# Optimization experiments

Hardware: AMD Instinct MI355X
Metric: run time of the kernel (lower is better)

The kernel has to match this reference:

```python
import jax, jax.numpy as jnp
import numpy as np

B, S, E = 2, 2048, 2048
NQ, NKV, HD = 16, 4, 128
WINDOW = 512
ROPE_BASE = 10000.0


def _rope(x):
    # x: [B, H, S, HD], interleaved even/odd rotation
    half = HD // 2
    freqs = 1.0 / (ROPE_BASE ** (2.0 * jnp.arange(half, dtype=jnp.float32) / HD))
    pos = jnp.arange(x.shape[2], dtype=jnp.float32)
    ang = pos[:, None] * freqs[None, :]            # [S, HD/2]
    cos = jnp.cos(ang)[None, None].astype(x.dtype)  # [1,1,S,HD/2]
    sin = jnp.sin(ang)[None, None].astype(x.dtype)
    xe = x[..., 0::2]
    xo = x[..., 1::2]
    re = xe * cos - xo * sin
    ro = xe * sin + xo * cos
    return jnp.stack([re, ro], axis=-1).reshape(x.shape)


def setup_inputs() -> dict:
    key = jax.random.key(0)
    ks = jax.random.split(key, 9)
    s_in = 1.0 / np.sqrt(E)
    s_out = 1.0 / np.sqrt(NQ * HD)
    return {
        "x": jax.random.normal(ks[0], (B, S, E), jnp.float32),
        "Wq": jax.random.normal(ks[1], (E, NQ * HD), jnp.float32) * s_in,
        "bq": jax.random.normal(ks[2], (NQ * HD,), jnp.float32) * 0.01,
        "Wk": jax.random.normal(ks[3], (E, NKV * HD), jnp.float32) * s_in,
        "bk": jax.random.normal(ks[4], (NKV * HD,), jnp.float32) * 0.01,
        "Wv": jax.random.normal(ks[5], (E, NKV * HD), jnp.float32) * s_in,
        "bv": jax.random.normal(ks[6], (NKV * HD,), jnp.float32) * 0.01,
        "Wo": jax.random.normal(ks[7], (NQ * HD, E), jnp.float32) * s_out,
        "bo": jax.random.normal(ks[8], (E,), jnp.float32) * 0.01,
    }


def reference(x, Wq, bq, Wk, bk, Wv, bv, Wo, bo):
    b, s, _ = x.shape
    q = (x @ Wq + bq).reshape(b, s, NQ, HD).transpose(0, 2, 1, 3)   # [B,NQ,S,HD]
    k = (x @ Wk + bk).reshape(b, s, NKV, HD).transpose(0, 2, 1, 3)  # [B,NKV,S,HD]
    v = (x @ Wv + bv).reshape(b, s, NKV, HD).transpose(0, 2, 1, 3)
    q = _rope(q)
    k = _rope(k)
    rep = NQ // NKV
    k = jnp.repeat(k, rep, axis=1)  # [B,NQ,S,HD], matches torch repeat pattern
    v = jnp.repeat(v, rep, axis=1)
    scores = jnp.einsum("bhqd,bhkd->bhqk", q, k) / np.sqrt(HD)
    i = jnp.arange(s)[:, None]
    j = jnp.arange(s)[None, :]
    allowed = (j <= i) & ((i - j) <= WINDOW)  # sliding-window causal mask
    scores = jnp.where(allowed[None, None], scores, -jnp.inf)
    weights = jax.nn.softmax(scores, axis=-1)
    out = jnp.einsum("bhqk,bhkd->bhqd", weights, v)
    out = out.transpose(0, 2, 1, 3).reshape(b, s, NQ * HD)
    return out @ Wo + bo
```

## Files before the change

### kernel.cpp

```cpp
#include <hip/hip_runtime.h>
#include <hip/hip_bf16.h>
#include <math.h>

#define BB 2
#define SS 2048
#define EE 2048
#define NQ 16
#define NKV 4
#define HD 128
#define WINDOW 512

typedef __hip_bfloat16 bf16;
typedef short short8 __attribute__((ext_vector_type(8)));
typedef float f32x4 __attribute__((ext_vector_type(4)));

__device__ __forceinline__ float toF(bf16 v) { return __bfloat162float(v); }
__device__ __forceinline__ bf16 toB(float v) { return __float2bfloat16(v); }

__device__ __forceinline__ void gld_lds16(const void* g, void* l) {
    __builtin_amdgcn_global_load_lds(
        (const __attribute__((address_space(1))) void*)g,
        (__attribute__((address_space(3))) void*)l, 16, 0, 0);
}

__global__ __launch_bounds__(256) void convert_bf16(const float* __restrict__ in,
                                                    bf16* __restrict__ out, int n) {
    int i = (blockIdx.x * 256 + threadIdx.x) * 4;
    if (i >= n) return;
    const float4 v = *(const float4*)(in + i);
    bf16 o[4] = {toB(v.x), toB(v.y), toB(v.z), toB(v.w)};
    *(uint2*)(out + i) = *(const uint2*)o;
}

__global__ __launch_bounds__(256) void convert_transpose(const float* __restrict__ in,
                                                         bf16* __restrict__ out,
                                                         int K, int N) {
    __shared__ float tile[32][33];
    const int t = threadIdx.x;
    const int tx = t & 31, ty = t >> 5;
    const int n0 = blockIdx.x * 32, k0 = blockIdx.y * 32;
#pragma unroll
    for (int r = 0; r < 4; r++)
        tile[ty + r * 8][tx] = in[(size_t)(k0 + ty + r * 8) * N + n0 + tx];
    __syncthreads();
#pragma unroll
    for (int r = 0; r < 4; r++)
        out[(size_t)(n0 + ty + r * 8) * K + k0 + tx] = toB(tile[tx][ty + r * 8]);
}

__global__ __launch_bounds__(256) void convert_transpose_qkv(
    const float* __restrict__ Wq, const float* __restrict__ Wk,
    const float* __restrict__ Wv, bf16* __restrict__ out) {
    __shared__ float tile[32][33];
    const int t = threadIdx.x;
    const int tx = t & 31, ty = t >> 5;
    const int n0 = blockIdx.x * 32, k0 = blockIdx.y * 32;
    const float* src; int N, nl0;
    if (n0 < 2048)      { src = Wq; N = 2048; nl0 = n0; }
    else if (n0 < 2560) { src = Wk; N = 512;  nl0 = n0 - 2048; }
    else                { src = Wv; N = 512;  nl0 = n0 - 2560; }
#pragma unroll
    for (int r = 0; r < 4; r++)
        tile[ty + r * 8][tx] = src[(size_t)(k0 + ty + r * 8) * N + nl0 + tx];
    __syncthreads();
#pragma unroll
    for (int r = 0; r < 4; r++)
        out[(size_t)(n0 + ty + r * 8) * 2048 + k0 + tx] = toB(tile[tx][ty + r * 8]);
}

__global__ __launch_bounds__(256) void v_transpose(const bf16* __restrict__ Vb,
                                                   bf16* __restrict__ Vtg) {
    __shared__ bf16 tile[64 * 72];
    const int t = threadIdx.x;
    const int s0 = blockIdx.x * 64;
    const int d0 = (blockIdx.y & 1) * 64;
    const int bh = blockIdx.y >> 1;
    const int b = bh >> 2, hkv = bh & 3;

    const bf16* src = Vb + (((size_t)b * SS + s0) * NKV + hkv) * HD + d0;
#pragma unroll
    for (int half = 0; half < 2; half++) {
        const int sl = (t >> 3) + half * 32;
        const int c  = t & 7;
        const int c2 = c ^ (sl & 7);
        short8 v = *(const short8*)(src + (size_t)sl * (NKV * HD) + c * 8);
        *(short8*)(&tile[sl * 72 + c2 * 8]) = v;
    }
    __syncthreads();

    const int d = t >> 2;
    const int sc = t & 3;
    bf16* dst = Vtg + (((size_t)b * NKV + hkv) * HD + d0 + d) * SS + s0 + sc * 16;
#pragma unroll
    for (int g = 0; g < 2; g++) {
        bf16 pk[8];
#pragma unroll
        for (int k = 0; k < 8; k++) {
            const int s = sc * 16 + g * 8 + k;
            const int c2 = (d >> 3) ^ (s & 7);
            pk[k] = tile[s * 72 + c2 * 8 + (d & 7)];
        }
        *(uint4*)(dst + g * 8) = *(const uint4*)pk;
    }
}

template <int MODE>
__global__ __launch_bounds__(256) void mfma_gemm(
    const bf16* __restrict__ A, const bf16* __restrict__ BT,
    const float* __restrict__ b0, const float* __restrict__ b1,
    const float* __restrict__ b2,
    float* __restrict__ Yf,
    bf16* __restrict__ Yq, bf16* __restrict__ Yk, bf16* __restrict__ Yv,
    int M, int N, int K) {
    __shared__ bf16 As[128 * 32];
    __shared__ bf16 Bs[128 * 32];

    const int t = threadIdx.x;
    const int lane = t & 63;
    const int w = t >> 6;
    const int wm = w >> 1, wn = w & 1;
    const int m0 = blockIdx.y * 128, n0 = blockIdx.x * 128;

    const int srow = lane >> 2;
    const int sg   = lane & 3;
    const int scol = (sg ^ ((srow >> 1) & 3)) * 8;

    f32x4 acc[4][4];
#pragma unroll
    for (int i = 0; i < 4; i++)
#pragma unroll
        for (int j = 0; j < 4; j++) acc[i][j] = (f32x4)0.f;

    const int lr = lane & 15;
    const int lq = lane >> 4;
    const int slotr = (lq ^ ((lr >> 1) & 3)) * 8;

    for (int k0 = 0; k0 < K; k0 += 32) {
#pragma unroll
        for (int s = 0; s < 2; s++) {
            const int c = w * 2 + s;
            gld_lds16(A + (size_t)(m0 + c * 16 + srow) * K + k0 + scol, As + c * 512);
            gld_lds16(BT + (size_t)(n0 + c * 16 + srow) * K + k0 + scol, Bs + c * 512);
        }
        __syncthreads();
        short8 af[4], bfv[4];
#pragma unroll
        for (int i = 0; i < 4; i++)
            af[i] = *(const short8*)(As + (wm * 64 + i * 16 + lr) * 32 + slotr);
#pragma unroll
        for (int j = 0; j < 4; j++)
            bfv[j] = *(const short8*)(Bs + (wn * 64 + j * 16 + lr) * 32 + slotr);
#pragma unroll
        for (int i = 0; i < 4; i++)
#pragma unroll
            for (int j = 0; j < 4; j++)
                acc[i][j] = __builtin_amdgcn_mfma_f32_16x16x32_bf16(af[i], bfv[j],
                                                                    acc[i][j], 0, 0, 0);
        __syncthreads();
    }

    if (MODE == 0) {
#pragma unroll
        for (int j = 0; j < 4; j++) {
            const int col = n0 + wn * 64 + j * 16 + lr;
            const float bj = b0[col];
#pragma unroll
            for (int i = 0; i < 4; i++) {
                const int row = m0 + wm * 64 + i * 16 + lq * 4;
#pragma unroll
                for (int r = 0; r < 4; r++)
                    Yf[(size_t)(row + r) * N + col] = acc[i][j][r] + bj;
            }
        }
    } else if (n0 < 2560) {
        bf16* outp; const float* bias; int ldc, c0; float oscale;
        if (n0 < 2048) { outp = Yq; bias = b0; ldc = 2048; c0 = n0;
                         oscale = 0.08838834764831845f; }
        else           { outp = Yk; bias = b1; ldc = 512;  c0 = n0 - 2048;
                         oscale = 1.0f; }
#pragma unroll
        for (int j = 0; j < 4; j++) {
            const int col = c0 + wn * 64 + j * 16 + lr;
            const float bj = bias[col];
            const int d2 = (col & 127) >> 1;
            const bool odd = col & 1;
            const float freq = __expf(-0.14384103622589045f * (float)d2);
#pragma unroll
            for (int i = 0; i < 4; i++) {
                const int row = m0 + wm * 64 + i * 16 + lq * 4;
#pragma unroll
                for (int r = 0; r < 4; r++) {
                    const float v = acc[i][j][r] + bj;
                    const float p = __shfl_xor(v, 1, 64);
                    const float ang = (float)((row + r) & (SS - 1)) * freq;
                    float sn, cs;
                    __sincosf(ang, &sn, &cs);
                    const float o = odd ? (p * sn + v * cs) : (v * cs - p * sn);
                    outp[(size_t)(row + r) * ldc + col] = toB(o * oscale);
                }
            }
        }
    } else {
        const int c0 = n0 - 2560;
#pragma unroll
        for (int j = 0; j < 4; j++) {
            const int col = c0 + wn * 64 + j * 16 + lr;
            const float bj = b2[col];
#pragma unroll
            for (int i = 0; i < 4; i++) {
                const int row = m0 + wm * 64 + i * 16 + lq * 4;
#pragma unroll
                for (int r = 0; r < 4; r++)
                    Yv[(size_t)(row + r) * 512 + col] = toB(acc[i][j][r] + bj);
            }
        }
    }
}

__global__ __launch_bounds__(256) void attn_mfma(const bf16* __restrict__ Q,
                                                 const bf16* __restrict__ K,
                                                 const bf16* __restrict__ Vt_g,
                                                 bf16* __restrict__ Oout) {
    __shared__ bf16 Ks[64 * 128];
    __shared__ bf16 Vt[128 * 64];
    __shared__ bf16 Ps[4 * 16 * 72];

    const int t = threadIdx.x;
    const int lane = t & 63;
    const int w = t >> 6;
    const int q0 = blockIdx.x * 64;
    const int h = blockIdx.y;
    const int b = blockIdx.z;
    const int hkv = h >> 2;
    const int lr = lane & 15;
    const int lq = lane >> 4;

    short8 aq[4];
    {
        const int q = q0 + w * 16 + lr;
        const bf16* qp = Q + (((size_t)b * SS + q) * NQ + h) * HD + lq * 8;
#pragma unroll
        for (int ks = 0; ks < 4; ks++) aq[ks] = *(const short8*)(qp + ks * 32);
    }

    f32x4 Oa[8];
#pragma unroll
    for (int nb = 0; nb < 8; nb++) Oa[nb] = (f32x4)0.f;
    float mprev[4] = {-3.0e38f, -3.0e38f, -3.0e38f, -3.0e38f};
    float lsum[4] = {0.f, 0.f, 0.f, 0.f};

    bf16* Pw = Ps + w * 16 * 72;
    const int jstart = (q0 >= WINDOW) ? (q0 - WINDOW) : 0;
    const bf16* Vrow = Vt_g + ((size_t)b * NKV + hkv) * HD * SS;

    for (int c0 = jstart; c0 <= q0; c0 += 64) {
        __syncthreads();
#pragma unroll
        for (int s = 0; s < 4; s++) {
            const int kr = w * 16 + s * 4 + (lane >> 4);
            const int sl = lane & 15;
            const int g = (sl & 8) | ((sl & 7) ^ (kr & 7));
            gld_lds16(K + (((size_t)b * SS + c0 + kr) * NKV + hkv) * HD + g * 8,
                      Ks + (w * 16 + s * 4) * 128);
        }
#pragma unroll
        for (int s = 0; s < 4; s++) {
            const int dr = w * 32 + s * 8 + (lane >> 3);
            const int sl = lane & 7;
            const int g = sl ^ (dr & 7);
            gld_lds16(Vrow + (size_t)dr * SS + c0 + g * 8,
                      Vt + (w * 32 + s * 8) * 64);
        }
        __syncthreads();

        f32x4 sa[4];
#pragma unroll
        for (int nb = 0; nb < 4; nb++) sa[nb] = (f32x4)0.f;
#pragma unroll
        for (int ks = 0; ks < 4; ks++) {
#pragma unroll
            for (int nb = 0; nb < 4; nb++) {
                const int row = nb * 16 + lr;
                const int g = ks * 4 + lq;
                const int slot = (g & 8) | ((g & 7) ^ (row & 7));
                short8 bk = *(const short8*)(Ks + row * 128 + slot * 8);
                sa[nb] = __builtin_amdgcn_mfma_f32_16x16x32_bf16(aq[ks], bk, sa[nb], 0, 0, 0);
            }
        }

        const int rowb = q0 + w * 16 + lq * 4;
        const bool needmask = !((c0 + 63 <= q0 + w * 16) &&
                                (q0 + w * 16 + 15 - c0 <= WINDOW));
        float pr[4][4], alpha[4];
#pragma unroll
        for (int r = 0; r < 4; r++) {
            const int row = rowb + r;
            float sv[4];
            float mx = -3.0e38f;
            if (needmask) {
#pragma unroll
                for (int nb = 0; nb < 4; nb++) {
                    const int col = c0 + nb * 16 + lr;
                    const bool valid = (col <= row) && (row - col <= WINDOW);
                    sv[nb] = valid ? sa[nb][r] : -3.0e38f;
                    mx = fmaxf(mx, sv[nb]);
                }
            } else {
#pragma unroll
                for (int nb = 0; nb < 4; nb++) {
                    sv[nb] = sa[nb][r];
                    mx = fmaxf(mx, sv[nb]);
                }
            }
#pragma unroll
            for (int off = 1; off < 16; off <<= 1) mx = fmaxf(mx, __shfl_xor(mx, off, 64));
            const float mn = fmaxf(fmaxf(mprev[r], mx), -1.0e30f);
            alpha[r] = __expf(mprev[r] - mn);
            mprev[r] = mn;
            float rs = 0.f;
#pragma unroll
            for (int nb = 0; nb < 4; nb++) {
                const float p = __expf(sv[nb] - mn);
                pr[r][nb] = p;
                rs += p;
            }
#pragma unroll
            for (int off = 1; off < 16; off <<= 1) rs += __shfl_xor(rs, off, 64);
            lsum[r] = lsum[r] * alpha[r] + rs;
        }

#pragma unroll
        for (int r = 0; r < 4; r++)
#pragma unroll
            for (int nb = 0; nb < 4; nb++)
                Pw[(lq * 4 + r) * 72 + nb * 16 + lr] = toB(pr[r][nb]);

#pragma unroll
        for (int nb = 0; nb < 8; nb++)
#pragma unroll
            for (int r = 0; r < 4; r++) Oa[nb][r] *= alpha[r];
#pragma unroll
        for (int ks = 0; ks < 2; ks++) {
            short8 pa = *(const short8*)(Pw + lr * 72 + ks * 32 + lq * 8);
#pragma unroll
            for (int nb = 0; nb < 8; nb++) {
                const int d = nb * 16 + lr;
                const int g = ks * 4 + lq;
                const int slot = g ^ (d & 7);
                short8 bv = *(const short8*)(Vt + d * 64 + slot * 8);
                Oa[nb] = __builtin_amdgcn_mfma_f32_16x16x32_bf16(pa, bv, Oa[nb], 0, 0, 0);
            }
        }
    }

    float linv[4];
#pragma unroll
    for (int r = 0; r < 4; r++) linv[r] = 1.f / lsum[r];
    const int rowb = q0 + w * 16 + lq * 4;
#pragma unroll
    for (int nb = 0; nb < 8; nb++)
#pragma unroll
        for (int r = 0; r < 4; r++)
            Oout[(((size_t)b * SS + rowb + r) * NQ + h) * HD + nb * 16 + lr] =
                toB(Oa[nb][r] * linv[r]);
}

extern "C" void kernel_launch(void* const* d_in, const int* in_sizes, int n_in,
                              void* d_out, int out_size, void* d_ws, size_t ws_size,
                              hipStream_t stream) {
    const float* x  = (const float*)d_in[0];
    const float* Wq = (const float*)d_in[1];
    const float* bq = (const float*)d_in[2];
    const float* Wk = (const float*)d_in[3];
    const float* bk = (const float*)d_in[4];
    const float* Wv = (const float*)d_in[5];
    const float* bv = (const float*)d_in[6];
    const float* Wo = (const float*)d_in[7];
    const float* bo = (const float*)d_in[8];
    float* out = (float*)d_out;

    const int M   = BB * SS;
    const int DQ  = NQ * HD;
    const int DKV = NKV * HD;
    const int NPK = DQ + 2 * DKV;

    bf16* xb     = (bf16*)d_ws;
    bf16* WqkvT  = xb + (size_t)M * EE;
    bf16* WoT    = WqkvT + (size_t)NPK * EE;
    bf16* Vb     = WoT;
    bf16* Qb     = WoT + (size_t)EE * DQ;
    bf16* Kb     = Qb + (size_t)M * DQ;
    bf16* Vtg    = Kb + (size_t)M * DKV;

    convert_bf16<<<(M * EE / 4 + 255) / 256, 256, 0, stream>>>(x, xb, M * EE);
    convert_transpose_qkv<<<dim3(NPK / 32, EE / 32), 256, 0, stream>>>(Wq, Wk, Wv, WqkvT);

    mfma_gemm<1><<<dim3(NPK / 128, M / 128), 256, 0, stream>>>(
        xb, WqkvT, bq, bk, bv, nullptr, Qb, Kb, Vb, M, NPK, EE);

    v_transpose<<<dim3(SS / 64, 2 * BB * NKV), 256, 0, stream>>>(Vb, Vtg);
    convert_transpose<<<dim3(DQ / 32, DQ / 32), 256, 0, stream>>>(Wo, WoT, DQ, EE);

    attn_mfma<<<dim3(SS / 64, NQ, BB), 256, 0, stream>>>(Qb, Kb, Vtg, Qb);

    mfma_gemm<0><<<dim3(EE / 128, M / 128), 256, 0, stream>>>(
        Qb, WoT, bo, nullptr, nullptr, out, nullptr, nullptr, nullptr, M, EE, DQ);
}
```

Before: 338.9 us.

## Use single-wave attention blocks reading K/V directly from global memory

The attention kernel changes from 256-thread blocks covering 64 query rows, which staged K and V tiles into shared memory with barriers, to 64-thread single-wavefront blocks covering 16 query rows. Each wave loads its K and V MFMA fragments straight from global memory, and the key-chunk start is aligned to 64. This removes __syncthreads and LDS staging and launches four times as many blocks for occupancy. In exchange, K/V reuse across the four waves is lost, so global/L2 traffic rises and the V fragment loads are strided.

Measured after the change: 463.5 us. 36.8% more time.

```diff
diff --git a/kernel.cpp b/kernel.cpp
--- a/kernel.cpp
+++ b/kernel.cpp
@@ -217,18 +217,14 @@
     }
 }
 
-__global__ __launch_bounds__(256) void attn_mfma(const bf16* __restrict__ Q,
-                                                 const bf16* __restrict__ K,
-                                                 const bf16* __restrict__ Vt_g,
-                                                 bf16* __restrict__ Oout) {
-    __shared__ bf16 Ks[64 * 128];
-    __shared__ bf16 Vt[128 * 64];
-    __shared__ bf16 Ps[4 * 16 * 72];
-
-    const int t = threadIdx.x;
-    const int lane = t & 63;
-    const int w = t >> 6;
-    const int q0 = blockIdx.x * 64;
+__global__ __launch_bounds__(64) void attn_mfma(const bf16* __restrict__ Q,
+                                                const bf16* __restrict__ K,
+                                                const bf16* __restrict__ Vt_g,
+                                                bf16* __restrict__ Oout) {
+    __shared__ bf16 Ps[16 * 72];
+
+    const int lane = threadIdx.x;
+    const int q0 = blockIdx.x * 16;
     const int h = blockIdx.y;
     const int b = blockIdx.z;
     const int hkv = h >> 2;
@@ -237,8 +233,7 @@
 
     short8 aq[4];
     {
-        const int q = q0 + w * 16 + lr;
-        const bf16* qp = Q + (((size_t)b * SS + q) * NQ + h) * HD + lq * 8;
+        const bf16* qp = Q + (((size_t)b * SS + q0 + lr) * NQ + h) * HD + lq * 8;
 #pragma unroll
         for (int ks = 0; ks < 4; ks++) aq[ks] = *(const short8*)(qp + ks * 32);
     }
@@ -249,48 +244,33 @@
     float mprev[4] = {-3.0e38f, -3.0e38f, -3.0e38f, -3.0e38f};
     float lsum[4] = {0.f, 0.f, 0.f, 0.f};
 
-    bf16* Pw = Ps + w * 16 * 72;
-    const int jstart = (q0 >= WINDOW) ? (q0 - WINDOW) : 0;
+    const bf16* Krow = K + ((size_t)b * SS * NKV + hkv) * HD;
     const bf16* Vrow = Vt_g + ((size_t)b * NKV + hkv) * HD * SS;
 
-    for (int c0 = jstart; c0 <= q0; c0 += 64) {
-        __syncthreads();
-#pragma unroll
-        for (int s = 0; s < 4; s++) {
-            const int kr = w * 16 + s * 4 + (lane >> 4);
-            const int sl = lane & 15;
-            const int g = (sl & 8) | ((sl & 7) ^ (kr & 7));
-            gld_lds16(K + (((size_t)b * SS + c0 + kr) * NKV + hkv) * HD + g * 8,
-                      Ks + (w * 16 + s * 4) * 128);
-        }
-#pragma unroll
-        for (int s = 0; s < 4; s++) {
-            const int dr = w * 32 + s * 8 + (lane >> 3);
-            const int sl = lane & 7;
-            const int g = sl ^ (dr & 7);
-            gld_lds16(Vrow + (size_t)dr * SS + c0 + g * 8,
-                      Vt + (w * 32 + s * 8) * 64);
-        }
-        __syncthreads();
-
+    int jstart = q0 - WINDOW;
+    if (jstart < 0) jstart = 0;
+    jstart &= ~63;
+
+    for (int c0 = jstart; c0 <= q0 + 15; c0 += 64) {
+        short8 bk[4][4];
+#pragma unroll
+        for (int nb = 0; nb < 4; nb++) {
+            const bf16* kp = Krow + (size_t)(c0 + nb * 16 + lr) * (NKV * HD) + lq * 8;
+#pragma unroll
+            for (int ks = 0; ks < 4; ks++) bk[ks][nb] = *(const short8*)(kp + ks * 32);
+        }
         f32x4 sa[4];
 #pragma unroll
         for (int nb = 0; nb < 4; nb++) sa[nb] = (f32x4)0.f;
 #pragma unroll
-        for (int ks = 0; ks < 4; ks++) {
-#pragma unroll
-            for (int nb = 0; nb < 4; nb++) {
-                const int row = nb * 16 + lr;
-                const int g = ks * 4 + lq;
-                const int slot = (g & 8) | ((g & 7) ^ (row & 7));
-                short8 bk = *(const short8*)(Ks + row * 128 + slot * 8);
-                sa[nb] = __builtin_amdgcn_mfma_f32_16x16x32_bf16(aq[ks], bk, sa[nb], 0, 0, 0);
-            }
-        }
-
-        const int rowb = q0 + w * 16 + lq * 4;
-        const bool needmask = !((c0 + 63 <= q0 + w * 16) &&
-                                (q0 + w * 16 + 15 - c0 <= WINDOW));
+        for (int ks = 0; ks < 4; ks++)
+#pragma unroll
+            for (int nb = 0; nb < 4; nb++)
+                sa[nb] = __builtin_amdgcn_mfma_f32_16x16x32_bf16(aq[ks], bk[ks][nb],
+                                                                 sa[nb], 0, 0, 0);
+
+        const int rowb = q0 + lq * 4;
+        const bool needmask = !((c0 + 63 <= q0) && (q0 + 15 - c0 <= WINDOW));
         float pr[4][4], alpha[4];
 #pragma unroll
         for (int r = 0; r < 4; r++) {
@@ -333,21 +313,19 @@
         for (int r = 0; r < 4; r++)
 #pragma unroll
             for (int nb = 0; nb < 4; nb++)
-                Pw[(lq * 4 + r) * 72 + nb * 16 + lr] = toB(pr[r][nb]);
+                Ps[(lq * 4 + r) * 72 + nb * 16 + lr] = toB(pr[r][nb]);
 
 #pragma unroll
         for (int nb = 0; nb < 8; nb++)
 #pragma unroll
             for (int r = 0; r < 4; r++) Oa[nb][r] *= alpha[r];
 #pragma unroll
-        for (int ks = 0; ks < 2; ks++) {
-            short8 pa = *(const short8*)(Pw + lr * 72 + ks * 32 + lq * 8);
+        for (int ks2 = 0; ks2 < 2; ks2++) {
+            short8 pa = *(const short8*)(Ps + lr * 72 + ks2 * 32 + lq * 8);
 #pragma unroll
             for (int nb = 0; nb < 8; nb++) {
-                const int d = nb * 16 + lr;
-                const int g = ks * 4 + lq;
-                const int slot = g ^ (d & 7);
-                short8 bv = *(const short8*)(Vt + d * 64 + slot * 8);
+                short8 bv = *(const short8*)(Vrow + (size_t)(nb * 16 + lr) * SS +
+                                             c0 + ks2 * 32 + lq * 8);
                 Oa[nb] = __builtin_amdgcn_mfma_f32_16x16x32_bf16(pa, bv, Oa[nb], 0, 0, 0);
             }
         }
@@ -356,7 +334,7 @@
     float linv[4];
 #pragma unroll
     for (int r = 0; r < 4; r++) linv[r] = 1.f / lsum[r];
-    const int rowb = q0 + w * 16 + lq * 4;
+    const int rowb = q0 + lq * 4;
 #pragma unroll
     for (int nb = 0; nb < 8; nb++)
 #pragma unroll
@@ -401,7 +379,7 @@
     v_transpose<<<dim3(SS / 64, 2 * BB * NKV), 256, 0, stream>>>(Vb, Vtg);
     convert_transpose<<<dim3(DQ / 32, DQ / 32), 256, 0, stream>>>(Wo, WoT, DQ, EE);
 
-    attn_mfma<<<dim3(SS / 64, NQ, BB), 256, 0, stream>>>(Qb, Kb, Vtg, Qb);
+    attn_mfma<<<dim3(SS / 16, NQ, BB), 64, 0, stream>>>(Qb, Kb, Vtg, Qb);
 
     mfma_gemm<0><<<dim3(EE / 128, M / 128), 256, 0, stream>>>(
         Qb, WoT, bo, nullptr, nullptr, out, nullptr, nullptr, nullptr, M, EE, DQ);
```

## Process 128 queries per attention block with two 16-row tiles per wave

Applied to the files above, without the earlier changes.

The attention kernel now handles 128 query rows per block, with each wave owning 32 rows as two 16-row MFMA tiles. Each K/V tile loaded into LDS is reused across twice as many queries, which roughly halves K/V global traffic and load/sync overhead per query. The cost is double the accumulator registers per wave, which can lower occupancy, and a grid half the size (512 blocks). Waves skip compute on chunks outside their own window, so they still join the shared loads but may sit idle for part of the loop.

Result: slower. 373.0 us (+10.1%).

```diff
diff --git a/kernel.cpp b/kernel.cpp
--- a/kernel.cpp
+++ b/kernel.cpp
@@ -223,37 +223,42 @@
                                                  bf16* __restrict__ Oout) {
     __shared__ bf16 Ks[64 * 128];
     __shared__ bf16 Vt[128 * 64];
-    __shared__ bf16 Ps[4 * 16 * 72];
+    __shared__ bf16 Ps[4 * 32 * 72];
 
     const int t = threadIdx.x;
     const int lane = t & 63;
     const int w = t >> 6;
-    const int q0 = blockIdx.x * 64;
+    const int q0 = blockIdx.x * 128;
     const int h = blockIdx.y;
     const int b = blockIdx.z;
     const int hkv = h >> 2;
     const int lr = lane & 15;
     const int lq = lane >> 4;
-
-    short8 aq[4];
-    {
-        const int q = q0 + w * 16 + lr;
-        const bf16* qp = Q + (((size_t)b * SS + q) * NQ + h) * HD + lq * 8;
-#pragma unroll
-        for (int ks = 0; ks < 4; ks++) aq[ks] = *(const short8*)(qp + ks * 32);
-    }
-
-    f32x4 Oa[8];
-#pragma unroll
-    for (int nb = 0; nb < 8; nb++) Oa[nb] = (f32x4)0.f;
-    float mprev[4] = {-3.0e38f, -3.0e38f, -3.0e38f, -3.0e38f};
-    float lsum[4] = {0.f, 0.f, 0.f, 0.f};
-
-    bf16* Pw = Ps + w * 16 * 72;
+    const int wq0 = q0 + w * 32;
+
+    short8 aq[2][4];
+#pragma unroll
+    for (int u = 0; u < 2; u++) {
+        const bf16* qp = Q + (((size_t)b * SS + wq0 + u * 16 + lr) * NQ + h) * HD + lq * 8;
+#pragma unroll
+        for (int ks = 0; ks < 4; ks++) aq[u][ks] = *(const short8*)(qp + ks * 32);
+    }
+
+    f32x4 Oa[2][8];
+#pragma unroll
+    for (int u = 0; u < 2; u++)
+#pragma unroll
+        for (int nb = 0; nb < 8; nb++) Oa[u][nb] = (f32x4)0.f;
+    float mprev[2][4], lsum[2][4];
+#pragma unroll
+    for (int u = 0; u < 2; u++)
+#pragma unroll
+        for (int r = 0; r < 4; r++) { mprev[u][r] = -3.0e38f; lsum[u][r] = 0.f; }
+
+    bf16* Pw = Ps + w * 32 * 72;
     const int jstart = (q0 >= WINDOW) ? (q0 - WINDOW) : 0;
-    const bf16* Vrow = Vt_g + ((size_t)b * NKV + hkv) * HD * SS;
-
-    for (int c0 = jstart; c0 <= q0; c0 += 64) {
+
+    for (int c0 = jstart; c0 < q0 + 128; c0 += 64) {
         __syncthreads();
 #pragma unroll
         for (int s = 0; s < 4; s++) {
@@ -268,14 +273,18 @@
             const int dr = w * 32 + s * 8 + (lane >> 3);
             const int sl = lane & 7;
             const int g = sl ^ (dr & 7);
-            gld_lds16(Vrow + (size_t)dr * SS + c0 + g * 8,
+            gld_lds16(Vt_g + (((size_t)b * NKV + hkv) * HD + dr) * SS + c0 + g * 8,
                       Vt + (w * 32 + s * 8) * 64);
         }
         __syncthreads();
 
-        f32x4 sa[4];
-#pragma unroll
-        for (int nb = 0; nb < 4; nb++) sa[nb] = (f32x4)0.f;
+        if (c0 > wq0 + 31 || c0 + 63 < wq0 - WINDOW) continue;
+
+        f32x4 sa[2][4];
+#pragma unroll
+        for (int u = 0; u < 2; u++)
+#pragma unroll
+            for (int nb = 0; nb < 4; nb++) sa[u][nb] = (f32x4)0.f;
 #pragma unroll
         for (int ks = 0; ks < 4; ks++) {
 #pragma unroll
@@ -284,85 +293,101 @@
                 const int g = ks * 4 + lq;
                 const int slot = (g & 8) | ((g & 7) ^ (row & 7));
                 short8 bk = *(const short8*)(Ks + row * 128 + slot * 8);
-                sa[nb] = __builtin_amdgcn_mfma_f32_16x16x32_bf16(aq[ks], bk, sa[nb], 0, 0, 0);
-            }
-        }
-
-        const int rowb = q0 + w * 16 + lq * 4;
-        const bool needmask = !((c0 + 63 <= q0 + w * 16) &&
-                                (q0 + w * 16 + 15 - c0 <= WINDOW));
-        float pr[4][4], alpha[4];
-#pragma unroll
-        for (int r = 0; r < 4; r++) {
-            const int row = rowb + r;
-            float sv[4];
-            float mx = -3.0e38f;
-            if (needmask) {
+                sa[0][nb] = __builtin_amdgcn_mfma_f32_16x16x32_bf16(aq[0][ks], bk,
+                                                                    sa[0][nb], 0, 0, 0);
+                sa[1][nb] = __builtin_amdgcn_mfma_f32_16x16x32_bf16(aq[1][ks], bk,
+                                                                    sa[1][nb], 0, 0, 0);
+            }
+        }
+
+        float alpha[2][4];
+#pragma unroll
+        for (int u = 0; u < 2; u++) {
+            const int rowb = wq0 + u * 16 + lq * 4;
+            const bool needmask = !((c0 + 63 <= wq0 + u * 16) &&
+                                    (wq0 + u * 16 + 15 - c0 <= WINDOW));
+            float pr[4][4];
+#pragma unroll
+            for (int r = 0; r < 4; r++) {
+                const int row = rowb + r;
+                float sv[4];
+                float mx = -3.0e38f;
+                if (needmask) {
+#pragma unroll
+                    for (int nb = 0; nb < 4; nb++) {
+                        const int col = c0 + nb * 16 + lr;
+                        const bool valid = (col <= row) && (row - col <= WINDOW);
+                        sv[nb] = valid ? sa[u][nb][r] : -3.0e38f;
+                        mx = fmaxf(mx, sv[nb]);
+                    }
+                } else {
+#pragma unroll
+                    for (int nb = 0; nb < 4; nb++) {
+                        sv[nb] = sa[u][nb][r];
+                        mx = fmaxf(mx, sv[nb]);
+                    }
+                }
+#pragma unroll
+                for (int off = 1; off < 16; off <<= 1)
+                    mx = fmaxf(mx, __shfl_xor(mx, off, 64));
+                const float mn = fmaxf(fmaxf(mprev[u][r], mx), -1.0e30f);
+                alpha[u][r] = __expf(mprev[u][r] - mn);
+                mprev[u][r] = mn;
+                float rs = 0.f;
 #pragma unroll
                 for (int nb = 0; nb < 4; nb++) {
-                    const int col = c0 + nb * 16 + lr;
-                    const bool valid = (col <= row) && (row - col <= WINDOW);
-                    sv[nb] = valid ? sa[nb][r] : -3.0e38f;
-                    mx = fmaxf(mx, sv[nb]);
+                    const float p = __expf(sv[nb] - mn);
+                    pr[r][nb] = p;
+                    rs += p;
                 }
-            } else {
-#pragma unroll
-                for (int nb = 0; nb < 4; nb++) {
-                    sv[nb] = sa[nb][r];
-                    mx = fmaxf(mx, sv[nb]);
-                }
-            }
-#pragma unroll
-            for (int off = 1; off < 16; off <<= 1) mx = fmaxf(mx, __shfl_xor(mx, off, 64));
-            const float mn = fmaxf(fmaxf(mprev[r], mx), -1.0e30f);
-            alpha[r] = __expf(mprev[r] - mn);
-            mprev[r] = mn;
-            float rs = 0.f;
-#pragma unroll
-            for (int nb = 0; nb < 4; nb++) {
-                const float p = __expf(sv[nb] - mn);
-                pr[r][nb] = p;
-                rs += p;
-            }
-#pragma unroll
-            for (int off = 1; off < 16; off <<= 1) rs += __shfl_xor(rs, off, 64);
-            lsum[r] = lsum[r] * alpha[r] + rs;
-        }
-
-#pragma unroll
-        for (int r = 0; r < 4; r++)
-#pragma unroll
-            for (int nb = 0; nb < 4; nb++)
-                Pw[(lq * 4 + r) * 72 + nb * 16 + lr] = toB(pr[r][nb]);
-
-#pragma unroll
-        for (int nb = 0; nb < 8; nb++)
-#pragma unroll
-            for (int r = 0; r < 4; r++) Oa[nb][r] *= alpha[r];
-#pragma unroll
-        for (int ks = 0; ks < 2; ks++) {
-            short8 pa = *(const short8*)(Pw + lr * 72 + ks * 32 + lq * 8);
+#pragma unroll
+                for (int off = 1; off < 16; off <<= 1) rs += __shfl_xor(rs, off, 64);
+                lsum[u][r] = lsum[u][r] * alpha[u][r] + rs;
+            }
+#pragma unroll
+            for (int r = 0; r < 4; r++)
+#pragma unroll
+                for (int nb = 0; nb < 4; nb++)
+                    Pw[(u * 16 + lq * 4 + r) * 72 + nb * 16 + lr] = toB(pr[r][nb]);
+        }
+
+#pragma unroll
+        for (int u = 0; u < 2; u++)
+#pragma unroll
+            for (int nb = 0; nb < 8; nb++)
+#pragma unroll
+                for (int r = 0; r < 4; r++) Oa[u][nb][r] *= alpha[u][r];
+#pragma unroll
+        for (int ks2 = 0; ks2 < 2; ks2++) {
+            short8 pa0 = *(const short8*)(Pw + lr * 72 + ks2 * 32 + lq * 8);
+            short8 pa1 = *(const short8*)(Pw + (16 + lr) * 72 + ks2 * 32 + lq * 8);
 #pragma unroll
             for (int nb = 0; nb < 8; nb++) {
                 const int d = nb * 16 + lr;
-                const int g = ks * 4 + lq;
+                const int g = ks2 * 4 + lq;
                 const int slot = g ^ (d & 7);
                 short8 bv = *(const short8*)(Vt + d * 64 + slot * 8);
-                Oa[nb] = __builtin_amdgcn_mfma_f32_16x16x32_bf16(pa, bv, Oa[nb], 0, 0, 0);
-            }
-        }
-    }
-
-    float linv[4];
-#pragma unroll
-    for (int r = 0; r < 4; r++) linv[r] = 1.f / lsum[r];
-    const int rowb = q0 + w * 16 + lq * 4;
-#pragma unroll
-    for (int nb = 0; nb < 8; nb++)
-#pragma unroll
-        for (int r = 0; r < 4; r++)
-            Oout[(((size_t)b * SS + rowb + r) * NQ + h) * HD + nb * 16 + lr] =
-                toB(Oa[nb][r] * linv[r]);
+                Oa[0][nb] = __builtin_amdgcn_mfma_f32_16x16x32_bf16(pa0, bv,
+                                                                    Oa[0][nb], 0, 0, 0);
+                Oa[1][nb] = __builtin_amdgcn_mfma_f32_16x16x32_bf16(pa1, bv,
+                                                                    Oa[1][nb], 0, 0, 0);
+            }
+        }
+    }
+
+#pragma unroll
+    for (int u = 0; u < 2; u++) {
+        float linv[4];
+#pragma unroll
+        for (int r = 0; r < 4; r++) linv[r] = 1.f / lsum[u][r];
+        const int rowb = wq0 + u * 16 + lq * 4;
+#pragma unroll
+        for (int nb = 0; nb < 8; nb++)
+#pragma unroll
+            for (int r = 0; r < 4; r++)
+                Oout[(((size_t)b * SS + rowb + r) * NQ + h) * HD + nb * 16 + lr] =
+                    toB(Oa[u][nb][r] * linv[r]);
+    }
 }
 
 extern "C" void kernel_launch(void* const* d_in, const int* in_sizes, int n_in,
@@ -401,7 +426,7 @@
     v_transpose<<<dim3(SS / 64, 2 * BB * NKV), 256, 0, stream>>>(Vb, Vtg);
     convert_transpose<<<dim3(DQ / 32, DQ / 32), 256, 0, stream>>>(Wo, WoT, DQ, EE);
 
-    attn_mfma<<<dim3(SS / 64, NQ, BB), 256, 0, stream>>>(Qb, Kb, Vtg, Qb);
+    attn_mfma<<<dim3(SS / 128, NQ, BB), 256, 0, stream>>>(Qb, Kb, Vtg, Qb);
 
     mfma_gemm<0><<<dim3(EE / 128, M / 128), 256, 0, stream>>>(
         Qb, WoT, bo, nullptr, nullptr, out, nullptr, nullptr, nullptr, M, EE, DQ);
```
